# Kernel tuning notes

Measured on AMD Instinct MI355X. Metric: run time of the kernel, lower is better.

The kernel has to match this reference:

```python
import jax, jax.numpy as jnp
import numpy as np

B, C, H, W = 8, 256, 32, 32
N_HEADS, CH = 8, 32          # channel_head = channels // num_heads
HID = N_HEADS * CH           # hidden_channels


def setup_inputs() -> dict:
    key = jax.random.key(0)
    k1, k2, k3 = jax.random.split(key, 3)
    return {
        "x": jax.random.normal(k1, (B, C, H, W), dtype=jnp.float32),
        "w_qkv": jax.random.normal(k2, (3 * HID, C), dtype=jnp.float32) * 0.02,
        "b_qkv": jnp.zeros((3 * HID,), dtype=jnp.float32),
        "w_out": jax.random.normal(k3, (C, HID), dtype=jnp.float32) * 0.02,
        "b_out": jnp.zeros((C,), dtype=jnp.float32),
    }


def reference(x, w_qkv, b_qkv, w_out, b_out):
    b, c, h, w = x.shape
    s = h * w
    # qkv_conv: 1x1 conv + SiLU (norm='none' inside Conv2dBlock)
    qkv = jnp.einsum('bchw,oc->bohw', x, w_qkv) + b_qkv[None, :, None, None]
    qkv = jax.nn.silu(qkv)
    # rearrange 'b (n c) h w -> b n (3*ch) s' then chunk into q,k,v
    qkv = qkv.reshape(b, N_HEADS, 3 * CH, s)
    q, k, v = jnp.split(qkv, 3, axis=2)          # each [b, n, ch, s]
    # scores over flattened spatial positions, scaled by sqrt(channel_head)
    scores = jnp.einsum('bncs,bnct->bnst', q, k) / jnp.sqrt(jnp.float32(CH))
    attn = jax.nn.softmax(scores, axis=-1)        # softmax over key positions
    out = jnp.einsum('bnst,bnct->bncs', attn, v)  # [b, n, ch, s]
    out = out.reshape(b, N_HEADS * CH, h, w)      # 'b n c h w -> b (n c) h w'
    # out_conv: 1x1 conv, activation='none'
    out = jnp.einsum('bchw,oc->bohw', out, w_out) + b_out[None, :, None, None]
    # skip_connect=True, norm='none' => identity
    return out + x
```

## Files before the change

kernel.cpp:

```cpp
#include <hip/hip_runtime.h>
#include <math.h>

#define BB   8
#define NHD  8
#define SSZ  1024
#define CIN  256
#define HIDC 256

typedef __bf16 bf16_t;
typedef bf16_t bf16x8 __attribute__((ext_vector_type(8)));
typedef float  f32x4v __attribute__((ext_vector_type(4)));

typedef __attribute__((address_space(3))) unsigned short as3_u16;
typedef __attribute__((address_space(1))) unsigned short as1_u16;

__device__ inline unsigned cvt_pk_bf16(float lo, float hi) {
    unsigned r;
    asm("v_cvt_pk_bf16_f32 %0, %1, %2" : "=v"(r) : "v"(lo), "v"(hi));
    return r;
}
__device__ inline unsigned short f2bf(float f) {
    unsigned u = __builtin_bit_cast(unsigned, f);
    u = (u + 0x7fffu + ((u >> 16) & 1u)) >> 16;
    return (unsigned short)u;
}
__device__ inline float exp2_fast(float x) {
    float r;
    asm("v_exp_f32 %0, %1" : "=v"(r) : "v"(x));
    return r;
}
__device__ inline int kmap5(int i) {
    return ((i >> 2) & 3) * 8 + ((i >> 4) & 1) * 4 + (i & 3);
}

#define QKV_LDS_LOAD(WF, XF, CB0)                                                   \
    {                                                                               \
        _Pragma("unroll") for (int df = 0; df < 2; ++df) {                          \
            const int orow = (w >> 1) * 32 + df * 16 + ln;                          \
            WF[df] = *(const bf16x8*)(Ws + orow * 256 + ((((CB0) + g) ^ (orow & 7)) << 3)); \
        }                                                                           \
        _Pragma("unroll") for (int sf = 0; sf < 4; ++sf) {                          \
            const int srow = sbl + sf * 16 + ln;                                    \
            XF[sf] = *(const bf16x8*)(Xs + srow * 128 + (((((CB0) & 15) + g) ^ (srow & 15)) << 3)); \
        }                                                                           \
    }
#define QKV_MMA(WF, XF)                                                             \
    {                                                                               \
        _Pragma("unroll") for (int df = 0; df < 2; ++df)                            \
            _Pragma("unroll") for (int sf = 0; sf < 4; ++sf)                        \
                acc[df][sf] = __builtin_amdgcn_mfma_f32_16x16x32_bf16(WF[df], XF[sf], acc[df][sf], 0, 0, 0); \
    }

__global__ __launch_bounds__(256) void qkv_fused(
    const float* __restrict__ W, const float* __restrict__ x,
    const float* __restrict__ w_out, const float* __restrict__ bias,
    unsigned short* __restrict__ qkT, unsigned short* __restrict__ v_buf,
    unsigned short* __restrict__ Wo)
{
    __shared__ unsigned short Ws[64 * 256];
    __shared__ unsigned short Xs[128 * 128];

    const int tid = threadIdx.x;

    if (blockIdx.y == 12) {
        const int chunk = blockIdx.z * 8 + blockIdx.x;
        const size_t idx = (size_t)chunk * 1024 + (size_t)tid * 4;
        float4 v = *(const float4*)(w_out + idx);
        ushort4 pk;
        pk.x = f2bf(v.x); pk.y = f2bf(v.y); pk.z = f2bf(v.z); pk.w = f2bf(v.w);
        *(ushort4*)(Wo + idx) = pk;
        return;
    }

    const int l = tid & 63, w = tid >> 6;
    const int g = l >> 4, ln = l & 15;
    const int b  = blockIdx.z;
    const int o0 = blockIdx.y * 64;
    const int ob = o0 + (w >> 1) * 32;
    const int s0 = blockIdx.x * 128;
    const int sbl = (w & 1) * 64;

    #pragma unroll
    for (int it = 0; it < 16; ++it) {
        const int u = it * 256 + tid;
        const int row = u >> 6;
        const int cq  = u & 63;
        const float4 v = *(const float4*)(W + (size_t)(o0 + row) * 256 + cq * 4);
        const int c  = cq * 4;
        const int cbp = ((c >> 3) ^ (row & 7)) << 3;
        unsigned two[2] = { cvt_pk_bf16(v.x, v.y), cvt_pk_bf16(v.z, v.w) };
        *(uint2*)(Ws + row * 256 + cbp + (c & 7)) = *(uint2*)two;
    }

    f32x4v acc[2][4];
    const f32x4v zero4 = {0.f, 0.f, 0.f, 0.f};
    #pragma unroll
    for (int df = 0; df < 2; ++df)
        #pragma unroll
        for (int sf = 0; sf < 4; ++sf) acc[df][sf] = zero4;

    bf16x8 wA[2], xA[4], wB[2], xB[4];

    #pragma unroll
    for (int h = 0; h < 2; ++h) {
        if (h) __syncthreads();
        #pragma unroll
        for (int it = 0; it < 8; ++it) {
            const int u  = it * 256 + tid;
            const int cp = u >> 5;
            const int sq = u & 31;
            const float* r0 = x + ((size_t)b * CIN + h * 128 + 2 * cp) * SSZ + s0 + sq * 4;
            const f32x4v a = *(const f32x4v*)r0;
            const f32x4v d = *(const f32x4v*)(r0 + SSZ);
            const int c_loc = 2 * cp;
            const int cb    = c_loc >> 3;
            #pragma unroll
            for (int j = 0; j < 4; ++j) {
                const int s_loc = sq * 4 + j;
                const int elem  = s_loc * 128 + ((cb ^ (s_loc & 15)) << 3) + (c_loc & 7);
                *(unsigned*)(Xs + elem) = cvt_pk_bf16(a[j], d[j]);
            }
        }
        __syncthreads();

        QKV_LDS_LOAD(wA, xA, h * 16 + 0);
        QKV_LDS_LOAD(wB, xB, h * 16 + 4);
        QKV_MMA(wA, xA);
        QKV_LDS_LOAD(wA, xA, h * 16 + 8);
        QKV_MMA(wB, xB);
        QKV_LDS_LOAD(wB, xB, h * 16 + 12);
        QKV_MMA(wA, xA);
        QKV_MMA(wB, xB);
    }

    #pragma unroll
    for (int df = 0; df < 2; ++df) {
        const int o16  = ob + df * 16;
        const int part = (o16 >> 5) % 3;
        const int head = o16 / 96;
        const int bh   = b * NHD + head;
        const float4 b4 = *(const float4*)(bias + o16 + g * 4);
        const float bias_r[4] = {b4.x, b4.y, b4.z, b4.w};
        const int chb = (o16 & 31) + g * 4;

        float vals[4][4];
        #pragma unroll
        for (int sf = 0; sf < 4; ++sf)
            #pragma unroll
            for (int r = 0; r < 4; ++r) {
                float z = acc[df][sf][r] + bias_r[r];
                z = z / (1.f + __expf(-z));
                if (part == 0) z *= 0.25503482107810536f;
                vals[sf][r] = z;
            }

        if (part < 2) {
            const int slotb = ((chb >> 2) & 3) * 8 + ((chb >> 4) & 1) * 4;
            #pragma unroll
            for (int sf = 0; sf < 4; ++sf) {
                const int key = s0 + sbl + sf * 16 + ln;
                ushort4 pk;
                pk.x = f2bf(vals[sf][0]); pk.y = f2bf(vals[sf][1]);
                pk.z = f2bf(vals[sf][2]); pk.w = f2bf(vals[sf][3]);
                *(ushort4*)(qkT + ((size_t)bh << 16) + (size_t)key * 64 + part * 32 + slotb) = pk;
            }
        } else {
            #pragma unroll
            for (int sf = 0; sf < 4; ++sf) {
                const int key  = s0 + sbl + sf * 16 + ln;
                const int koff = (key & ~31) + kmap5(key & 31);
                #pragma unroll
                for (int r = 0; r < 4; ++r)
                    v_buf[((size_t)bh << 15) + ((size_t)(chb + r) << 10) + koff] = f2bf(vals[sf][r]);
            }
        }
    }
}

__global__ __launch_bounds__(256) void attn_mfma(
    const unsigned short* __restrict__ qkT,
    const unsigned short* __restrict__ v_buf,
    unsigned short* __restrict__ At)
{
    __shared__ unsigned short Ksh[4][2048];
    __shared__ unsigned short Vsh[4][2048];

    const int tid = threadIdx.x;
    const int l   = tid & 63;
    const int w   = tid >> 6;
    const int g   = l >> 4;
    const int ln  = l & 15;
    const int bh  = blockIdx.x;
    const int qt  = blockIdx.y;

    const unsigned short* qkrow = qkT   + ((size_t)bh << 16);
    const unsigned short* vb    = v_buf + ((size_t)bh << 15);

    const int q0 = qt * 64 + w * 16;

    const bf16x8 qf_ = *(const bf16x8*)(qkrow + (size_t)(q0 + ln) * 64 + g * 8);

    const bf16x8 ones = __builtin_bit_cast(bf16x8,
        make_uint4(0x3F803F80u, 0x3F803F80u, 0x3F803F80u, 0x3F803F80u));

    f32x4v O_[2], lacc;
    const f32x4v zero4 = {0.f, 0.f, 0.f, 0.f};
    O_[0] = zero4; O_[1] = zero4; lacc = zero4;

    const int krow = tid >> 2, ksl = tid & 3;
    const int vrow = tid >> 3, vsl = tid & 7;
    const unsigned short* gk_base = qkrow + (size_t)krow * 64 + 32 + ((ksl ^ ((krow >> 1) & 3)) << 3);
    const unsigned short* gv_base = vb + ((size_t)vrow << 10) + ((vsl ^ (vrow & 7)) << 3);
    const int wbase = w << 9;

#define STAGE_KV(BUF, T0)                                                          \
    {                                                                              \
        __builtin_amdgcn_global_load_lds((const as1_u16*)(gk_base + (size_t)(T0) * 64), \
                                         (as3_u16*)&Ksh[BUF][wbase], 16, 0, 0);    \
        __builtin_amdgcn_global_load_lds((const as1_u16*)(gv_base + (T0)),         \
                                         (as3_u16*)&Vsh[BUF][wbase], 16, 0, 0);    \
    }

    auto compute = [&](int cur) {
        const unsigned short* Kb = &Ksh[cur][0];
        const unsigned short* Vb = &Vsh[cur][0];
        bf16x8 kf_[4], vf_[2][2];
        #pragma unroll
        for (int kf = 0; kf < 4; ++kf)
            kf_[kf] = *(const bf16x8*)(Kb + ((kf * 16 + ln) << 5) + ((g ^ ((ln >> 1) & 3)) << 3));
        #pragma unroll
        for (int df = 0; df < 2; ++df)
            #pragma unroll
            for (int kb = 0; kb < 2; ++kb)
                vf_[df][kb] = *(const bf16x8*)(Vb + ((df * 16 + ln) << 6) + ((((kb << 2) + g) ^ (ln & 7)) << 3));

        f32x4v s_[4];
        __builtin_amdgcn_s_setprio(1);
        #pragma unroll
        for (int kf = 0; kf < 4; ++kf)
            s_[kf] = __builtin_amdgcn_mfma_f32_16x16x32_bf16(kf_[kf], qf_, zero4, 0, 0, 0);
        __builtin_amdgcn_s_setprio(0);

        #pragma unroll
        for (int kf = 0; kf < 4; ++kf)
            #pragma unroll
            for (int r = 0; r < 4; ++r)
                s_[kf][r] = exp2_fast(s_[kf][r]);

        __builtin_amdgcn_s_setprio(1);
        #pragma unroll
        for (int kb = 0; kb < 2; ++kb) {
            unsigned w0 = cvt_pk_bf16(s_[2 * kb][0],     s_[2 * kb][1]);
            unsigned w1 = cvt_pk_bf16(s_[2 * kb][2],     s_[2 * kb][3]);
            unsigned w2 = cvt_pk_bf16(s_[2 * kb + 1][0], s_[2 * kb + 1][1]);
            unsigned w3 = cvt_pk_bf16(s_[2 * kb + 1][2], s_[2 * kb + 1][3]);
            bf16x8 pf = __builtin_bit_cast(bf16x8, make_uint4(w0, w1, w2, w3));
            lacc = __builtin_amdgcn_mfma_f32_16x16x32_bf16(ones, pf, lacc, 0, 0, 0);
            #pragma unroll
            for (int df = 0; df < 2; ++df)
                O_[df] = __builtin_amdgcn_mfma_f32_16x16x32_bf16(vf_[df][kb], pf, O_[df], 0, 0, 0);
        }
        __builtin_amdgcn_s_setprio(0);
    };

    STAGE_KV(0, 0);
    STAGE_KV(1, 64);
    #pragma unroll
    for (int t = 0; t < 14; ++t) {
        STAGE_KV((t + 2) & 3, (t + 2) * 64);
        asm volatile("s_waitcnt vmcnt(4)" ::: "memory");
        __builtin_amdgcn_s_barrier();
        asm volatile("" ::: "memory");
        compute(t & 3);
        asm volatile("" ::: "memory");
    }
    asm volatile("s_waitcnt vmcnt(2)" ::: "memory");
    __builtin_amdgcn_s_barrier();
    asm volatile("" ::: "memory");
    compute(2);
    asm volatile("" ::: "memory");
    asm volatile("s_waitcnt vmcnt(0)" ::: "memory");
    __builtin_amdgcn_s_barrier();
    asm volatile("" ::: "memory");
    compute(3);

    const int b = bh >> 3, n = bh & 7;
    unsigned short* Ab = At + ((size_t)b << 18);
    const float inv = 1.f / lacc[0];
    const int qpos = q0 + ln;
    #pragma unroll
    for (int df = 0; df < 2; ++df) {
        ushort4 pk;
        pk.x = f2bf(O_[df][0] * inv);
        pk.y = f2bf(O_[df][1] * inv);
        pk.z = f2bf(O_[df][2] * inv);
        pk.w = f2bf(O_[df][3] * inv);
        *(ushort4*)(Ab + (size_t)qpos * 256 + n * 32 + df * 16 + g * 4) = pk;
    }
}

#define OUT_LOAD(WF, AF, KK)                                                        \
    {                                                                               \
        _Pragma("unroll") for (int df = 0; df < 2; ++df)                            \
            WF[df] = *(const bf16x8*)(Wo + (size_t)(ob + df * 16 + ln) * 256 + (KK) + g * 8); \
        _Pragma("unroll") for (int sf = 0; sf < 2; ++sf)                            \
            AF[sf] = *(const bf16x8*)(Ab + (size_t)(sb + sf * 16 + ln) * 256 + (KK) + g * 8); \
    }
#define OUT_MMA(WF, AF)                                                             \
    {                                                                               \
        _Pragma("unroll") for (int df = 0; df < 2; ++df)                            \
            _Pragma("unroll") for (int sf = 0; sf < 2; ++sf)                        \
                acc[df][sf] = __builtin_amdgcn_mfma_f32_16x16x32_bf16(WF[df], AF[sf], acc[df][sf], 0, 0, 0); \
    }

__global__ __launch_bounds__(256) void out_mfma(
    const unsigned short* __restrict__ Wo, const unsigned short* __restrict__ At,
    const float* __restrict__ bias, const float* __restrict__ x,
    float* __restrict__ out)
{
    const int tid = threadIdx.x;
    const int l = tid & 63, w = tid >> 6;
    const int g = l >> 4, ln = l & 15;
    const int b  = blockIdx.z;
    const int ob = blockIdx.y * 32;
    const int sb = blockIdx.x * 128 + w * 32;

    const unsigned short* Ab = At + ((size_t)b << 18);

    f32x4v acc[2][2];
    const f32x4v zero4 = {0.f, 0.f, 0.f, 0.f};
    #pragma unroll
    for (int df = 0; df < 2; ++df)
        #pragma unroll
        for (int sf = 0; sf < 2; ++sf) acc[df][sf] = zero4;

    bf16x8 wA[2], aA[2], wB[2], aB[2];
    OUT_LOAD(wA, aA, 0);
    #pragma unroll
    for (int k0 = 0; k0 < 256; k0 += 64) {
        if (k0 + 32 < 256) OUT_LOAD(wB, aB, k0 + 32);
        OUT_MMA(wA, aA);
        if (k0 + 64 < 256) OUT_LOAD(wA, aA, k0 + 64);
        OUT_MMA(wB, aB);
    }

    #pragma unroll
    for (int df = 0; df < 2; ++df) {
        const float4 b4 = *(const float4*)(bias + ob + df * 16 + g * 4);
        const float bias_r[4] = {b4.x, b4.y, b4.z, b4.w};
        #pragma unroll
        for (int sf = 0; sf < 2; ++sf) {
            const int s = sb + sf * 16 + ln;
            #pragma unroll
            for (int r = 0; r < 4; ++r) {
                const int o = ob + df * 16 + g * 4 + r;
                const size_t idx = ((size_t)b * CIN + o) * SSZ + s;
                out[idx] = acc[df][sf][r] + bias_r[r] + x[idx];
            }
        }
    }
}

extern "C" void kernel_launch(void* const* d_in, const int* in_sizes, int n_in,
                              void* d_out, int out_size, void* d_ws, size_t ws_size,
                              hipStream_t stream)
{
    const float* x     = (const float*)d_in[0];
    const float* w_qkv = (const float*)d_in[1];
    const float* b_qkv = (const float*)d_in[2];
    const float* w_out = (const float*)d_in[3];
    const float* b_out = (const float*)d_in[4];
    float* out = (float*)d_out;

    unsigned short* qkT   = (unsigned short*)d_ws;
    unsigned short* v_buf = qkT   + ((size_t)64 << 16);
    unsigned short* At    = v_buf + ((size_t)64 << 15);
    unsigned short* Wo    = At    + ((size_t)8 << 18);

    qkv_fused<<<dim3(8, 13, 8), 256, 0, stream>>>(w_qkv, x, w_out, b_qkv, qkT, v_buf, Wo);
    attn_mfma<<<dim3(64, 16),   256, 0, stream>>>(qkT, v_buf, At);
    out_mfma <<<dim3(8, 8, 8),  256, 0, stream>>>(Wo, At, b_out, x, out);
}
```

Before: 52.54 us.

## Enlarge QKV output tile to 128 rows and attention query tile to 128

```diff
diff --git a/kernel.cpp b/kernel.cpp
--- a/kernel.cpp
+++ b/kernel.cpp
@@ -33,20 +33,20 @@
     return ((i >> 2) & 3) * 8 + ((i >> 4) & 1) * 4 + (i & 3);
 }
 
-#define QKV_LDS_LOAD(WF, XF, CB0)                                                   \
+#define QKV_LDS_LOAD(WF, XF, KB)                                                    \
     {                                                                               \
-        _Pragma("unroll") for (int df = 0; df < 2; ++df) {                          \
-            const int orow = (w >> 1) * 32 + df * 16 + ln;                          \
-            WF[df] = *(const bf16x8*)(Ws + orow * 256 + ((((CB0) + g) ^ (orow & 7)) << 3)); \
+        _Pragma("unroll") for (int df = 0; df < 4; ++df) {                          \
+            const int orow = (w >> 1) * 64 + df * 16 + ln;                          \
+            WF[df] = *(const bf16x8*)(Ws + orow * 128 + ((((KB) + g) ^ (orow & 15)) << 3)); \
         }                                                                           \
         _Pragma("unroll") for (int sf = 0; sf < 4; ++sf) {                          \
             const int srow = sbl + sf * 16 + ln;                                    \
-            XF[sf] = *(const bf16x8*)(Xs + srow * 128 + (((((CB0) & 15) + g) ^ (srow & 15)) << 3)); \
+            XF[sf] = *(const bf16x8*)(Xs + srow * 128 + ((((KB) + g) ^ (srow & 15)) << 3)); \
         }                                                                           \
     }
 #define QKV_MMA(WF, XF)                                                             \
     {                                                                               \
-        _Pragma("unroll") for (int df = 0; df < 2; ++df)                            \
+        _Pragma("unroll") for (int df = 0; df < 4; ++df)                            \
             _Pragma("unroll") for (int sf = 0; sf < 4; ++sf)                        \
                 acc[df][sf] = __builtin_amdgcn_mfma_f32_16x16x32_bf16(WF[df], XF[sf], acc[df][sf], 0, 0, 0); \
     }
@@ -57,12 +57,12 @@
     unsigned short* __restrict__ qkT, unsigned short* __restrict__ v_buf,
     unsigned short* __restrict__ Wo)
 {
-    __shared__ unsigned short Ws[64 * 256];
+    __shared__ unsigned short Ws[128 * 128];
     __shared__ unsigned short Xs[128 * 128];
 
     const int tid = threadIdx.x;
 
-    if (blockIdx.y == 12) {
+    if (blockIdx.y == 6) {
         const int chunk = blockIdx.z * 8 + blockIdx.x;
         const size_t idx = (size_t)chunk * 1024 + (size_t)tid * 4;
         float4 v = *(const float4*)(w_out + idx);
@@ -75,35 +75,34 @@
     const int l = tid & 63, w = tid >> 6;
     const int g = l >> 4, ln = l & 15;
     const int b  = blockIdx.z;
-    const int o0 = blockIdx.y * 64;
-    const int ob = o0 + (w >> 1) * 32;
+    const int o0 = blockIdx.y * 128;
+    const int ob = o0 + (w >> 1) * 64;
     const int s0 = blockIdx.x * 128;
     const int sbl = (w & 1) * 64;
 
-    #pragma unroll
-    for (int it = 0; it < 16; ++it) {
-        const int u = it * 256 + tid;
-        const int row = u >> 6;
-        const int cq  = u & 63;
-        const float4 v = *(const float4*)(W + (size_t)(o0 + row) * 256 + cq * 4);
-        const int c  = cq * 4;
-        const int cbp = ((c >> 3) ^ (row & 7)) << 3;
-        unsigned two[2] = { cvt_pk_bf16(v.x, v.y), cvt_pk_bf16(v.z, v.w) };
-        *(uint2*)(Ws + row * 256 + cbp + (c & 7)) = *(uint2*)two;
-    }
-
-    f32x4v acc[2][4];
+    f32x4v acc[4][4];
     const f32x4v zero4 = {0.f, 0.f, 0.f, 0.f};
     #pragma unroll
-    for (int df = 0; df < 2; ++df)
+    for (int df = 0; df < 4; ++df)
         #pragma unroll
         for (int sf = 0; sf < 4; ++sf) acc[df][sf] = zero4;
 
-    bf16x8 wA[2], xA[4], wB[2], xB[4];
+    bf16x8 wA[4], xA[4], wB[4], xB[4];
 
     #pragma unroll
     for (int h = 0; h < 2; ++h) {
         if (h) __syncthreads();
+        #pragma unroll
+        for (int it = 0; it < 16; ++it) {
+            const int u   = it * 256 + tid;
+            const int row = u >> 5;
+            const int cq  = u & 31;
+            const float4 v = *(const float4*)(W + (size_t)(o0 + row) * 256 + h * 128 + cq * 4);
+            const int c_loc = cq * 4;
+            const int cbp   = ((c_loc >> 3) ^ (row & 15)) << 3;
+            unsigned two[2] = { cvt_pk_bf16(v.x, v.y), cvt_pk_bf16(v.z, v.w) };
+            *(uint2*)(Ws + row * 128 + cbp + (c_loc & 7)) = *(uint2*)two;
+        }
         #pragma unroll
         for (int it = 0; it < 8; ++it) {
             const int u  = it * 256 + tid;
@@ -123,18 +122,18 @@
         }
         __syncthreads();
 
-        QKV_LDS_LOAD(wA, xA, h * 16 + 0);
-        QKV_LDS_LOAD(wB, xB, h * 16 + 4);
+        QKV_LDS_LOAD(wA, xA, 0);
+        QKV_LDS_LOAD(wB, xB, 4);
         QKV_MMA(wA, xA);
-        QKV_LDS_LOAD(wA, xA, h * 16 + 8);
+        QKV_LDS_LOAD(wA, xA, 8);
         QKV_MMA(wB, xB);
-        QKV_LDS_LOAD(wB, xB, h * 16 + 12);
+        QKV_LDS_LOAD(wB, xB, 12);
         QKV_MMA(wA, xA);
         QKV_MMA(wB, xB);
     }
 
     #pragma unroll
-    for (int df = 0; df < 2; ++df) {
+    for (int df = 0; df < 4; ++df) {
         const int o16  = ob + df * 16;
         const int part = (o16 >> 5) % 3;
         const int head = o16 / 96;
@@ -196,16 +195,23 @@
     const unsigned short* qkrow = qkT   + ((size_t)bh << 16);
     const unsigned short* vb    = v_buf + ((size_t)bh << 15);
 
-    const int q0 = qt * 64 + w * 16;
-
-    const bf16x8 qf_ = *(const bf16x8*)(qkrow + (size_t)(q0 + ln) * 64 + g * 8);
+    const int q0 = qt * 128 + w * 32;
+
+    bf16x8 qf_[2];
+    #pragma unroll
+    for (int qf = 0; qf < 2; ++qf)
+        qf_[qf] = *(const bf16x8*)(qkrow + (size_t)(q0 + qf * 16 + ln) * 64 + g * 8);
 
     const bf16x8 ones = __builtin_bit_cast(bf16x8,
         make_uint4(0x3F803F80u, 0x3F803F80u, 0x3F803F80u, 0x3F803F80u));
 
-    f32x4v O_[2], lacc;
+    f32x4v O_[2][2], lacc[2];
     const f32x4v zero4 = {0.f, 0.f, 0.f, 0.f};
-    O_[0] = zero4; O_[1] = zero4; lacc = zero4;
+    #pragma unroll
+    for (int df = 0; df < 2; ++df)
+        #pragma unroll
+        for (int qf = 0; qf < 2; ++qf) O_[df][qf] = zero4;
+    lacc[0] = zero4; lacc[1] = zero4;
 
     const int krow = tid >> 2, ksl = tid & 3;
     const int vrow = tid >> 3, vsl = tid & 7;
@@ -234,33 +240,36 @@
             for (int kb = 0; kb < 2; ++kb)
                 vf_[df][kb] = *(const bf16x8*)(Vb + ((df * 16 + ln) << 6) + ((((kb << 2) + g) ^ (ln & 7)) << 3));
 
-        f32x4v s_[4];
-        __builtin_amdgcn_s_setprio(1);
-        #pragma unroll
-        for (int kf = 0; kf < 4; ++kf)
-            s_[kf] = __builtin_amdgcn_mfma_f32_16x16x32_bf16(kf_[kf], qf_, zero4, 0, 0, 0);
-        __builtin_amdgcn_s_setprio(0);
-
-        #pragma unroll
-        for (int kf = 0; kf < 4; ++kf)
-            #pragma unroll
-            for (int r = 0; r < 4; ++r)
-                s_[kf][r] = exp2_fast(s_[kf][r]);
-
-        __builtin_amdgcn_s_setprio(1);
-        #pragma unroll
-        for (int kb = 0; kb < 2; ++kb) {
-            unsigned w0 = cvt_pk_bf16(s_[2 * kb][0],     s_[2 * kb][1]);
-            unsigned w1 = cvt_pk_bf16(s_[2 * kb][2],     s_[2 * kb][3]);
-            unsigned w2 = cvt_pk_bf16(s_[2 * kb + 1][0], s_[2 * kb + 1][1]);
-            unsigned w3 = cvt_pk_bf16(s_[2 * kb + 1][2], s_[2 * kb + 1][3]);
-            bf16x8 pf = __builtin_bit_cast(bf16x8, make_uint4(w0, w1, w2, w3));
-            lacc = __builtin_amdgcn_mfma_f32_16x16x32_bf16(ones, pf, lacc, 0, 0, 0);
-            #pragma unroll
-            for (int df = 0; df < 2; ++df)
-                O_[df] = __builtin_amdgcn_mfma_f32_16x16x32_bf16(vf_[df][kb], pf, O_[df], 0, 0, 0);
-        }
-        __builtin_amdgcn_s_setprio(0);
+        #pragma unroll
+        for (int qf = 0; qf < 2; ++qf) {
+            f32x4v s_[4];
+            __builtin_amdgcn_s_setprio(1);
+            #pragma unroll
+            for (int kf = 0; kf < 4; ++kf)
+                s_[kf] = __builtin_amdgcn_mfma_f32_16x16x32_bf16(kf_[kf], qf_[qf], zero4, 0, 0, 0);
+            __builtin_amdgcn_s_setprio(0);
+
+            #pragma unroll
+            for (int kf = 0; kf < 4; ++kf)
+                #pragma unroll
+                for (int r = 0; r < 4; ++r)
+                    s_[kf][r] = exp2_fast(s_[kf][r]);
+
+            __builtin_amdgcn_s_setprio(1);
+            #pragma unroll
+            for (int kb = 0; kb < 2; ++kb) {
+                unsigned w0 = cvt_pk_bf16(s_[2 * kb][0],     s_[2 * kb][1]);
+                unsigned w1 = cvt_pk_bf16(s_[2 * kb][2],     s_[2 * kb][3]);
+                unsigned w2 = cvt_pk_bf16(s_[2 * kb + 1][0], s_[2 * kb + 1][1]);
+                unsigned w3 = cvt_pk_bf16(s_[2 * kb + 1][2], s_[2 * kb + 1][3]);
+                bf16x8 pf = __builtin_bit_cast(bf16x8, make_uint4(w0, w1, w2, w3));
+                lacc[qf] = __builtin_amdgcn_mfma_f32_16x16x32_bf16(ones, pf, lacc[qf], 0, 0, 0);
+                #pragma unroll
+                for (int df = 0; df < 2; ++df)
+                    O_[df][qf] = __builtin_amdgcn_mfma_f32_16x16x32_bf16(vf_[df][kb], pf, O_[df][qf], 0, 0, 0);
+            }
+            __builtin_amdgcn_s_setprio(0);
+        }
     };
 
     STAGE_KV(0, 0);
@@ -286,16 +295,19 @@
 
     const int b = bh >> 3, n = bh & 7;
     unsigned short* Ab = At + ((size_t)b << 18);
-    const float inv = 1.f / lacc[0];
-    const int qpos = q0 + ln;
-    #pragma unroll
-    for (int df = 0; df < 2; ++df) {
-        ushort4 pk;
-        pk.x = f2bf(O_[df][0] * inv);
-        pk.y = f2bf(O_[df][1] * inv);
-        pk.z = f2bf(O_[df][2] * inv);
-        pk.w = f2bf(O_[df][3] * inv);
-        *(ushort4*)(Ab + (size_t)qpos * 256 + n * 32 + df * 16 + g * 4) = pk;
+    #pragma unroll
+    for (int qf = 0; qf < 2; ++qf) {
+        const float inv = 1.f / lacc[qf][0];
+        const int qpos = q0 + qf * 16 + ln;
+        #pragma unroll
+        for (int df = 0; df < 2; ++df) {
+            ushort4 pk;
+            pk.x = f2bf(O_[df][qf][0] * inv);
+            pk.y = f2bf(O_[df][qf][1] * inv);
+            pk.z = f2bf(O_[df][qf][2] * inv);
+            pk.w = f2bf(O_[df][qf][3] * inv);
+            *(ushort4*)(Ab + (size_t)qpos * 256 + n * 32 + df * 16 + g * 4) = pk;
+        }
     }
 }
 
@@ -377,7 +389,7 @@
     unsigned short* At    = v_buf + ((size_t)64 << 15);
     unsigned short* Wo    = At    + ((size_t)8 << 18);
 
-    qkv_fused<<<dim3(8, 13, 8), 256, 0, stream>>>(w_qkv, x, w_out, b_qkv, qkT, v_buf, Wo);
-    attn_mfma<<<dim3(64, 16),   256, 0, stream>>>(qkT, v_buf, At);
-    out_mfma <<<dim3(8, 8, 8),  256, 0, stream>>>(Wo, At, b_out, x, out);
-}
+    qkv_fused<<<dim3(8, 7, 8), 256, 0, stream>>>(w_qkv, x, w_out, b_qkv, qkT, v_buf, Wo);
+    attn_mfma<<<dim3(64, 8),   256, 0, stream>>>(qkT, v_buf, At);
+    out_mfma <<<dim3(8, 8, 8), 256, 0, stream>>>(Wo, At, b_out, x, out);
+}
```

New measurement: 55.68 us. +6.0%, slower.
